# Kernel tuning notes

Hardware: AMD Instinct MI355X
Metric: run time of the kernel (lower is better)

## Reference

```python
import jax, jax.numpy as jnp
import numpy as np

B, T, D = 2, 1024, 2048
N, K, H = 16, 4, 128          # num_heads, num_kv_heads, head_dim
TC = 1024                     # cached tokens
S = TC + T
MAX_WAVELENGTH = 10000.0
BIG_NEG = -2.3819763e38


def _apply_rope(x, positions):
    """RoPE: positions [B,L] applied to x [B,L,heads,H]."""
    half = x.shape[-1] // 2
    freq_exponents = (2.0 / x.shape[-1]) * jnp.arange(half, dtype=jnp.float32)
    timescale = MAX_WAVELENGTH ** freq_exponents                      # [H/2]
    radians = (positions.astype(jnp.float32)[..., None] / timescale)[..., None, :]  # [B,L,1,H/2]
    sin, cos = jnp.sin(radians), jnp.cos(radians)
    x1, x2 = jnp.split(x, 2, axis=-1)
    res = jnp.concatenate([x1 * cos - x2 * sin, x2 * cos + x1 * sin], axis=-1)
    return res.astype(x.dtype)


def setup_inputs() -> dict:
    key = jax.random.key(0)
    ks = jax.random.split(key, 8)
    x = jax.random.normal(ks[0], (B, T, D), dtype=jnp.float32)
    # new tokens sit right after the cache
    positions = jnp.broadcast_to(TC + jnp.arange(T, dtype=jnp.int32), (B, T))
    # causal mask over [cache + new]: query t may attend to keys s <= TC + t
    s_idx = jnp.arange(S)[None, :]
    t_idx = jnp.arange(T)[:, None]
    attn_mask = jnp.broadcast_to((s_idx <= TC + t_idx)[None, None, :, :], (B, 1, T, S))
    cache_k = jax.random.normal(ks[1], (B, TC, K, H), dtype=jnp.float32)
    cache_v = jax.random.normal(ks[2], (B, TC, K, H), dtype=jnp.float32)
    # lecun-normal-ish fan-in scaling (fan_in = D for projections, N*H for output)
    w_q = jax.random.normal(ks[3], (N, D, H), dtype=jnp.float32) * (D ** -0.5)
    w_kv = jax.random.normal(ks[4], (2, K, D, H), dtype=jnp.float32) * (D ** -0.5)
    w_out = jax.random.normal(ks[5], (N, H, D), dtype=jnp.float32) * ((N * H) ** -0.5)
    return {"x": x, "positions": positions, "attn_mask": attn_mask,
            "cache_k": cache_k, "cache_v": cache_v,
            "w_q": w_q, "w_kv": w_kv, "w_out": w_out}


def reference(x, positions, attn_mask, cache_k, cache_v, w_q, w_kv, w_out):
    dtype = x.dtype
    # projections (GQA path: num_kv_heads != num_heads)
    q = jnp.einsum('BTD,NDH->BTNH', x, w_q.astype(dtype))
    kv = jnp.einsum('BSD,CKDH->CBSKH', x, w_kv.astype(dtype))
    k_new, v_new = kv[0], kv[1]
    # inline RoPE + query scaling
    q = _apply_rope(q, positions) * (H ** -0.5)
    k_new = _apply_rope(k_new, positions)
    # KV-cache concat
    k = jnp.concatenate([cache_k, k_new], axis=1)   # [B,S,K,H]
    v = jnp.concatenate([cache_v, v_new], axis=1)
    # group heads: B T (K G) H -> B T K G H
    G = N // K
    qg = q.reshape(q.shape[0], q.shape[1], K, G, H)
    logits = jnp.einsum('BTKGH,BSKH->BKGTS', qg, k,
                        preferred_element_type=jnp.float32)
    masked = jnp.where(attn_mask[:, :, None, :, :], logits, BIG_NEG)
    probs = jax.nn.softmax(masked, axis=-1).astype(dtype)
    enc = jnp.einsum('BKGTS,BSKH->BTKGH', probs, v)
    enc = enc.reshape(enc.shape[0], enc.shape[1], N, H)  # B T (K G) H
    out = jnp.einsum('BTNH,NHD->BTD', enc, w_out.astype(dtype))
    return out, k, v
```

## Files before the change

### kernel.cpp

```cpp
#include <hip/hip_runtime.h>

#define B_  2
#define T_  1024
#define D_  2048
#define NH  16
#define KH  4
#define HD  128
#define TC_ 1024
#define S_  2048

typedef __bf16 bf16x4v __attribute__((ext_vector_type(4)));
typedef __bf16 bf16x8v __attribute__((ext_vector_type(8)));
typedef float  f32x4v  __attribute__((ext_vector_type(4)));

__device__ __forceinline__ void async_copy16(void* lds, const void* g) {
    __builtin_amdgcn_global_load_lds(
        (__attribute__((address_space(1))) void*)g,
        (__attribute__((address_space(3))) void*)lds, 16, 0, 0);
}

__global__ void cvt_x(const float* __restrict__ x, __bf16* __restrict__ xb) {
    int i = (blockIdx.x * 256 + threadIdx.x) * 4;
    float4 v = *(const float4*)(x + i);
    bf16x4v o; o[0]=(__bf16)v.x; o[1]=(__bf16)v.y; o[2]=(__bf16)v.z; o[3]=(__bf16)v.w;
    *(bf16x4v*)(xb + i) = o;
}

__global__ void tp_w(const float* __restrict__ in, __bf16* __restrict__ out) {
    __shared__ float tile[32][33];
    int h0 = blockIdx.x * 32;
    int d0 = blockIdx.y * 32;
    const float* ip = in + (size_t)blockIdx.z * (D_ * HD);
    __bf16* op = out + (size_t)blockIdx.z * (D_ * HD);
    int tx = threadIdx.x, ty = threadIdx.y;
    for (int i = 0; i < 32; i += 8)
        tile[ty + i][tx] = ip[(size_t)(d0 + ty + i) * HD + h0 + tx];
    __syncthreads();
    for (int i = 0; i < 32; i += 8)
        op[(size_t)(h0 + ty + i) * D_ + d0 + tx] = (__bf16)tile[tx][ty + i];
}

__global__ void tp_wout(const float* __restrict__ in, __bf16* __restrict__ out) {
    __shared__ float tile[32][33];
    int d0 = blockIdx.x * 32;
    int h0 = blockIdx.y * 32;
    int n  = blockIdx.z;
    const float* ip = in + (size_t)n * (HD * D_);
    int tx = threadIdx.x, ty = threadIdx.y;
    for (int i = 0; i < 32; i += 8)
        tile[ty + i][tx] = ip[(size_t)(h0 + ty + i) * D_ + d0 + tx];
    __syncthreads();
    for (int i = 0; i < 32; i += 8)
        out[(size_t)(d0 + ty + i) * (NH * HD) + n * HD + h0 + tx] = (__bf16)tile[tx][ty + i];
}

__global__ void tp_v(const float* __restrict__ vout, __bf16* __restrict__ vtb) {
    __shared__ float tile[32][33];
    int z = blockIdx.z; int b = z / KH, kh = z % KH;
    int h0 = blockIdx.x * 32;
    int s0 = blockIdx.y * 32;
    const float* ip = vout + ((size_t)b * S_ * KH + kh) * HD;
    int tx = threadIdx.x, ty = threadIdx.y;
    for (int i = 0; i < 32; i += 8)
        tile[ty + i][tx] = ip[(size_t)(s0 + ty + i) * (KH * HD) + h0 + tx];
    __syncthreads();
    __bf16* op = vtb + ((size_t)b * KH + kh) * (size_t)HD * S_;
    for (int i = 0; i < 32; i += 8)
        op[(size_t)(h0 + ty + i) * S_ + s0 + tx] = (__bf16)tile[tx][ty + i];
}

__global__ void copy_cache(const float4* __restrict__ ck, const float4* __restrict__ cv,
                           float* __restrict__ kout, float* __restrict__ vout,
                           __bf16* __restrict__ kb) {
    int i = blockIdx.x * 256 + threadIdx.x;
    int b = i >> 17;
    int r = i & 131071;
    float4 kv = ck[i];
    ((float4*)(kout + (size_t)b * S_ * KH * HD))[r] = kv;
    ((float4*)(vout + (size_t)b * S_ * KH * HD))[r] = cv[i];
    int h4 = r & 31;
    int kh = (r >> 5) & 3;
    int s  = r >> 7;
    bf16x4v o; o[0]=(__bf16)kv.x; o[1]=(__bf16)kv.y; o[2]=(__bf16)kv.z; o[3]=(__bf16)kv.w;
    *(bf16x4v*)(kb + (((size_t)(b * KH + kh) * S_ + s) * HD) + h4 * 4) = o;
}

__global__ __launch_bounds__(256, 2)
void gemm_bt(const __bf16* __restrict__ A, const __bf16* __restrict__ BT,
             float* __restrict__ C0, float* __restrict__ C1, int ldc, int kchunk) {
    __shared__ __bf16 As[128 * 64];
    __shared__ __bf16 Bs[128 * 64];
    const int m0 = blockIdx.x * 128, n0 = blockIdx.y * 128;
    const int kbeg = blockIdx.z * kchunk;
    float* C = blockIdx.z ? C1 : C0;
    const int tid = threadIdx.x;
    const int wave = tid >> 6, lane = tid & 63;
    const int quad = lane >> 4, l16 = lane & 15;
    const int wm = (wave & 1) * 64, wn = (wave >> 1) * 64;
    const int lrow = lane >> 3;
    const int lsw  = (lane & 7) ^ (lrow & 7);

    f32x4v acc[4][4];
    for (int i = 0; i < 4; i++)
        for (int j = 0; j < 4; j++)
            acc[i][j] = (f32x4v){0.f, 0.f, 0.f, 0.f};

    const __bf16* Abase = A + (size_t)m0 * D_;
    const __bf16* Bbase = BT + (size_t)n0 * D_;

    for (int k0 = kbeg; k0 < kbeg + kchunk; k0 += 64) {
        for (int j = 0; j < 4; j++) {
            int r = wave * 32 + j * 8;
            async_copy16(As + (size_t)r * 64,
                         Abase + (size_t)(r + lrow) * D_ + k0 + lsw * 8);
            async_copy16(Bs + (size_t)r * 64,
                         Bbase + (size_t)(r + lrow) * D_ + k0 + lsw * 8);
        }
        __syncthreads();
        for (int ks = 0; ks < 2; ks++) {
            const int ch = ((ks * 4 + quad) ^ (l16 & 7)) * 8;
            bf16x8v a[4], b[4];
            for (int i = 0; i < 4; i++)
                a[i] = *(const bf16x8v*)(As + (wm + i * 16 + l16) * 64 + ch);
            for (int j = 0; j < 4; j++)
                b[j] = *(const bf16x8v*)(Bs + (wn + j * 16 + l16) * 64 + ch);
            for (int i = 0; i < 4; i++)
                for (int j = 0; j < 4; j++)
                    acc[i][j] = __builtin_amdgcn_mfma_f32_16x16x32_bf16(a[i], b[j], acc[i][j], 0, 0, 0);
        }
        __syncthreads();
    }
    for (int i = 0; i < 4; i++)
        for (int j = 0; j < 4; j++)
            for (int r = 0; r < 4; r++) {
                int row = m0 + wm + i * 16 + quad * 4 + r;
                int col = n0 + wn + j * 16 + l16;
                C[(size_t)row * ldc + col] = acc[i][j][r];
            }
}

__global__ void add2(float* __restrict__ out, const float* __restrict__ p1) {
    int i = blockIdx.x * 256 + threadIdx.x;
    f32x4v a = *(const f32x4v*)(out + (size_t)i * 4);
    f32x4v b = *(const f32x4v*)(p1 + (size_t)i * 4);
    a[0]+=b[0]; a[1]+=b[1]; a[2]+=b[2]; a[3]+=b[3];
    *(f32x4v*)(out + (size_t)i * 4) = a;
}

__global__ void finish_rope(const float* __restrict__ proj, const int* __restrict__ pos,
                            __bf16* __restrict__ qws, float* __restrict__ kout,
                            float* __restrict__ vout, __bf16* __restrict__ kb) {
    const int tau = blockIdx.x;
    const int b = tau >> 10, t = tau & 1023;
    const float p = (float)pos[tau];
    const float* pr  = proj + (size_t)tau * 3072;
    const float* pr2 = pr + (size_t)2048 * 3072;
    const float qscale = 0.08838834764831845f;
    for (int idx = threadIdx.x; idx < (NH + KH) * 64; idx += 256) {
        int head = idx >> 6;
        int hh = idx & 63;
        float ang = p * __expf(-(float)hh * (9.210340371976184f / 64.0f));
        float sn, cs;
        __sincosf(ang, &sn, &cs);
        if (head < NH) {
            float x1 = pr[head * HD + hh]      + pr2[head * HD + hh];
            float x2 = pr[head * HD + hh + 64] + pr2[head * HD + hh + 64];
            size_t qo = ((size_t)tau * NH + head) * HD;
            qws[qo + hh]      = (__bf16)((x1 * cs - x2 * sn) * qscale);
            qws[qo + hh + 64] = (__bf16)((x2 * cs + x1 * sn) * qscale);
        } else {
            int kh = head - NH;
            float x1 = pr[2048 + kh * HD + hh]      + pr2[2048 + kh * HD + hh];
            float x2 = pr[2048 + kh * HD + hh + 64] + pr2[2048 + kh * HD + hh + 64];
            float k1 = x1 * cs - x2 * sn, k2 = x2 * cs + x1 * sn;
            size_t ko = ((size_t)(b * S_ + TC_ + t) * KH + kh) * HD;
            kout[ko + hh]      = k1;
            kout[ko + hh + 64] = k2;
            size_t kbo = ((size_t)(b * KH + kh) * S_ + TC_ + t) * HD;
            kb[kbo + hh]      = (__bf16)k1;
            kb[kbo + hh + 64] = (__bf16)k2;
        }
    }
    for (int idx = threadIdx.x; idx < KH * HD; idx += 256) {
        int kh = idx >> 7, h = idx & 127;
        vout[((size_t)(b * S_ + TC_ + t) * KH + kh) * HD + h] =
            pr[2560 + kh * HD + h] + pr2[2560 + kh * HD + h];
    }
}

__global__ __launch_bounds__(512, 1)
void attn(const __bf16* __restrict__ qws, const __bf16* __restrict__ kb,
          const __bf16* __restrict__ vtb, __bf16* __restrict__ enc) {
    __shared__ __bf16 Qs[128 * 128];
    __shared__ __bf16 Ks[128 * 128];
    __shared__ __bf16 Vs[128 * 128];
    __shared__ __bf16 Ps[128 * 128];

    const int t0 = blockIdx.x * 128;
    const int n  = blockIdx.y;
    const int b  = blockIdx.z;
    const int kh = n / (NH / KH);
    const int tid = threadIdx.x, wave = tid >> 6, lane = tid & 63;
    const int quad = lane >> 4, l16 = lane & 15;
    const int wm = wave * 16;
    const int arow = lane >> 4;
    const int acol = lane & 15;

    {
        const __bf16* qtile = qws + ((size_t)(b * T_ + t0) * NH + n) * HD;
        for (int jj = 0; jj < 4; jj++) {
            int r0 = wm + jj * 4;
            int row = r0 + arow;
            async_copy16(Qs + (size_t)r0 * 128,
                         qtile + (size_t)row * (NH * HD) + ((acol ^ (row & 15)) * 8));
        }
    }

    float m_run[4], l_run[4];
    f32x4v o_acc[8];
    for (int r = 0; r < 4; r++) { m_run[r] = -INFINITY; l_run[r] = 0.f; }
    for (int j = 0; j < 8; j++) o_acc[j] = (f32x4v){0.f, 0.f, 0.f, 0.f};

    const int nS = (TC_ + t0 + 128) >> 7;
    const __bf16* kbase = kb  + ((size_t)(b * KH + kh)) * S_ * HD;
    const __bf16* vbase = vtb + ((size_t)(b * KH + kh)) * (size_t)HD * S_;

    for (int st = 0; st < nS; st++) {
        const int s0 = st * 128;
        {
            const __bf16* ktile = kbase + (size_t)s0 * HD;
            for (int jj = 0; jj < 4; jj++) {
                int r0 = wm + jj * 4;
                int row = r0 + arow;
                async_copy16(Ks + (size_t)r0 * 128,
                             ktile + (size_t)row * HD + ((acol ^ (row & 15)) * 8));
            }
        }
        {
            const __bf16* vtile = vbase + s0;
            for (int jj = 0; jj < 4; jj++) {
                int r0 = wm + jj * 4;
                int row = r0 + arow;
                async_copy16(Vs + (size_t)r0 * 128,
                             vtile + (size_t)row * S_ + ((acol ^ (row & 15)) * 8));
            }
        }
        __syncthreads();

        f32x4v sc[8];
        for (int j = 0; j < 8; j++) sc[j] = (f32x4v){0.f, 0.f, 0.f, 0.f};
        for (int ks = 0; ks < 4; ks++) {
            int ch = (ks * 4 + quad) ^ l16;
            bf16x8v a = *(const bf16x8v*)(Qs + (wm + l16) * 128 + ch * 8);
            bf16x8v bb[8];
            for (int j = 0; j < 8; j++)
                bb[j] = *(const bf16x8v*)(Ks + (j * 16 + l16) * 128 + ch * 8);
            for (int j = 0; j < 8; j++)
                sc[j] = __builtin_amdgcn_mfma_f32_16x16x32_bf16(a, bb[j], sc[j], 0, 0, 0);
        }

        if (st == nS - 1) {
            for (int j = 0; j < 8; j++)
                for (int r = 0; r < 4; r++) {
                    int row = wm + quad * 4 + r;
                    int col = j * 16 + l16;
                    if (col > row) sc[j][r] = -3.0e38f;
                }
        }

        for (int r = 0; r < 4; r++) {
            float mx = sc[0][r];
            for (int j = 1; j < 8; j++) mx = fmaxf(mx, sc[j][r]);
            for (int off = 8; off >= 1; off >>= 1) mx = fmaxf(mx, __shfl_xor(mx, off, 64));
            mx = fmaxf(mx, m_run[r]);
            float alpha = __expf(m_run[r] - mx);
            m_run[r] = mx;
            float s = 0.f;
            for (int j = 0; j < 8; j++) {
                float pv = __expf(sc[j][r] - mx);
                sc[j][r] = pv;
                s += pv;
            }
            for (int off = 8; off >= 1; off >>= 1) s += __shfl_xor(s, off, 64);
            l_run[r] = l_run[r] * alpha + s;
            for (int j = 0; j < 8; j++) o_acc[j][r] *= alpha;
        }

        for (int j = 0; j < 8; j++)
            for (int r = 0; r < 4; r++) {
                int row = wm + quad * 4 + r;
                int c = (j * 2 + (l16 >> 3)) ^ (row & 15);
                Ps[row * 128 + c * 8 + (l16 & 7)] = (__bf16)sc[j][r];
            }
        __syncthreads();

        for (int ks = 0; ks < 4; ks++) {
            int ch = (ks * 4 + quad) ^ l16;
            bf16x8v a = *(const bf16x8v*)(Ps + (wm + l16) * 128 + ch * 8);
            bf16x8v bb[8];
            for (int j = 0; j < 8; j++)
                bb[j] = *(const bf16x8v*)(Vs + (j * 16 + l16) * 128 + ch * 8);
            for (int j = 0; j < 8; j++)
                o_acc[j] = __builtin_amdgcn_mfma_f32_16x16x32_bf16(a, bb[j], o_acc[j], 0, 0, 0);
        }
        __syncthreads();
    }

    for (int r = 0; r < 4; r++) {
        float inv = 1.0f / l_run[r];
        int row = wm + quad * 4 + r;
        for (int j = 0; j < 8; j++) {
            int col = j * 16 + l16;
            enc[((size_t)(b * T_ + t0 + row) * NH + n) * HD + col] =
                (__bf16)(o_acc[j][r] * inv);
        }
    }
}

extern "C" void kernel_launch(void* const* d_in, const int* in_sizes, int n_in,
                              void* d_out, int out_size, void* d_ws, size_t ws_size,
                              hipStream_t stream) {
    const float* x       = (const float*)d_in[0];
    const int*   pos     = (const int*)d_in[1];
    const float* cache_k = (const float*)d_in[3];
    const float* cache_v = (const float*)d_in[4];
    const float* w_q     = (const float*)d_in[5];
    const float* w_kv    = (const float*)d_in[6];
    const float* w_out   = (const float*)d_in[7];

    float* out  = (float*)d_out;
    float* kout = out  + (size_t)B_ * T_ * D_;
    float* vout = kout + (size_t)B_ * S_ * KH * HD;

    char* ws = (char*)d_ws;
    __bf16* xb   = (__bf16*)ws;  ws += (size_t)B_ * T_ * D_ * 2;
    __bf16* wt   = (__bf16*)ws;  ws += (size_t)3072 * D_ * 2;
    __bf16* wot  = (__bf16*)ws;  ws += (size_t)D_ * NH * HD * 2;
    float*  proj = (float*)ws;   ws += (size_t)2 * B_ * T_ * 3072 * 4;
    __bf16* qws  = (__bf16*)ws;  ws += (size_t)B_ * T_ * NH * HD * 2;
    __bf16* kbuf = (__bf16*)ws;  ws += (size_t)B_ * S_ * KH * HD * 2;
    __bf16* vtb  = (__bf16*)ws;  ws += (size_t)B_ * S_ * KH * HD * 2;
    __bf16* enc  = (__bf16*)ws;
    float*  proj1 = proj + (size_t)2048 * 3072;
    float*  op1   = proj;

    cvt_x<<<4096, 256, 0, stream>>>(x, xb);
    tp_w<<<dim3(4, 64, 16), dim3(32, 8), 0, stream>>>(w_q, wt);
    tp_w<<<dim3(4, 64, 8),  dim3(32, 8), 0, stream>>>(w_kv, wt + (size_t)16 * HD * D_);
    tp_wout<<<dim3(64, 4, 16), dim3(32, 8), 0, stream>>>(w_out, wot);
    copy_cache<<<1024, 256, 0, stream>>>((const float4*)cache_k, (const float4*)cache_v, kout, vout, kbuf);
    gemm_bt<<<dim3(16, 24, 2), 256, 0, stream>>>(xb, wt, proj, proj1, 3072, 1024);
    finish_rope<<<2048, 256, 0, stream>>>(proj, pos, qws, kout, vout, kbuf);
    tp_v<<<dim3(4, 64, 8), dim3(32, 8), 0, stream>>>(vout, vtb);
    attn<<<dim3(8, 16, 2), 512, 0, stream>>>(qws, kbuf, vtb, enc);
    gemm_bt<<<dim3(16, 16, 2), 256, 0, stream>>>(enc, wot, out, op1, 2048, 1024);
    add2<<<4096, 256, 0, stream>>>(out, op1);
}
```

Before: 280.0 us.

## Fuse QKV projection GEMM with RoPE epilogue, drop split-K partial buffers

```diff
diff --git a/kernel.cpp b/kernel.cpp
--- a/kernel.cpp
+++ b/kernel.cpp
@@ -86,6 +86,110 @@
 }
 
 __global__ __launch_bounds__(256, 2)
+void gemm_qkv(const __bf16* __restrict__ A, const __bf16* __restrict__ BT,
+              const int* __restrict__ pos, __bf16* __restrict__ qws,
+              float* __restrict__ kout, float* __restrict__ vout,
+              __bf16* __restrict__ kb) {
+    __shared__ __bf16 As[128 * 64];
+    __shared__ __bf16 Bs[128 * 64];
+    const int m0 = blockIdx.x * 128, n0 = blockIdx.y * 128;
+    const int tid = threadIdx.x;
+    const int wave = tid >> 6, lane = tid & 63;
+    const int quad = lane >> 4, l16 = lane & 15;
+    const int wm = (wave & 1) * 64;
+    const int bn0 = (wave >> 1) * 32;
+    const int lrow = lane >> 3;
+    const int lsw  = (lane & 7) ^ (lrow & 7);
+
+    f32x4v acc[4][4];
+    for (int i = 0; i < 4; i++)
+        for (int j = 0; j < 4; j++)
+            acc[i][j] = (f32x4v){0.f, 0.f, 0.f, 0.f};
+
+    const __bf16* Abase = A + (size_t)m0 * D_;
+    const __bf16* Bbase = BT + (size_t)n0 * D_;
+
+    for (int k0 = 0; k0 < D_; k0 += 64) {
+        for (int j = 0; j < 4; j++) {
+            int r = wave * 32 + j * 8;
+            async_copy16(As + (size_t)r * 64,
+                         Abase + (size_t)(r + lrow) * D_ + k0 + lsw * 8);
+            async_copy16(Bs + (size_t)r * 64,
+                         Bbase + (size_t)(r + lrow) * D_ + k0 + lsw * 8);
+        }
+        __syncthreads();
+        for (int ks = 0; ks < 2; ks++) {
+            const int ch = ((ks * 4 + quad) ^ (l16 & 7)) * 8;
+            bf16x8v a[4], b[4];
+            for (int i = 0; i < 4; i++)
+                a[i] = *(const bf16x8v*)(As + (wm + i * 16 + l16) * 64 + ch);
+            for (int j = 0; j < 4; j++) {
+                int bn = bn0 + (j >> 1) * 16 + (j & 1) * 64;
+                b[j] = *(const bf16x8v*)(Bs + (bn + l16) * 64 + ch);
+            }
+            for (int i = 0; i < 4; i++)
+                for (int j = 0; j < 4; j++)
+                    acc[i][j] = __builtin_amdgcn_mfma_f32_16x16x32_bf16(a[i], b[j], acc[i][j], 0, 0, 0);
+        }
+        __syncthreads();
+    }
+
+    const float RFREQ = 9.210340371976184f / 64.0f;
+    const float qscale = 0.08838834764831845f;
+    const int head = blockIdx.y;
+
+    if (head < NH) {
+        for (int i = 0; i < 4; i++)
+            for (int r = 0; r < 4; r++) {
+                int row = m0 + wm + i * 16 + quad * 4 + r;
+                float p = (float)pos[row];
+                size_t qo = ((size_t)row * NH + head) * HD;
+                for (int jp = 0; jp < 2; jp++) {
+                    int hh = bn0 + jp * 16 + l16;
+                    float ang = p * __expf(-(float)hh * RFREQ);
+                    float sn, cs; __sincosf(ang, &sn, &cs);
+                    float x1 = acc[i][jp * 2][r], x2 = acc[i][jp * 2 + 1][r];
+                    qws[qo + hh]      = (__bf16)((x1 * cs - x2 * sn) * qscale);
+                    qws[qo + hh + 64] = (__bf16)((x2 * cs + x1 * sn) * qscale);
+                }
+            }
+    } else if (head < NH + KH) {
+        int kh = head - NH;
+        for (int i = 0; i < 4; i++)
+            for (int r = 0; r < 4; r++) {
+                int row = m0 + wm + i * 16 + quad * 4 + r;
+                int b = row >> 10, t = row & 1023;
+                float p = (float)pos[row];
+                size_t ko  = ((size_t)(b * S_ + TC_ + t) * KH + kh) * HD;
+                size_t kbo = ((size_t)(b * KH + kh) * S_ + TC_ + t) * HD;
+                for (int jp = 0; jp < 2; jp++) {
+                    int hh = bn0 + jp * 16 + l16;
+                    float ang = p * __expf(-(float)hh * RFREQ);
+                    float sn, cs; __sincosf(ang, &sn, &cs);
+                    float x1 = acc[i][jp * 2][r], x2 = acc[i][jp * 2 + 1][r];
+                    float k1 = x1 * cs - x2 * sn, k2 = x2 * cs + x1 * sn;
+                    kout[ko + hh]      = k1;
+                    kout[ko + hh + 64] = k2;
+                    kb[kbo + hh]      = (__bf16)k1;
+                    kb[kbo + hh + 64] = (__bf16)k2;
+                }
+            }
+    } else {
+        int kh = head - NH - KH;
+        for (int i = 0; i < 4; i++)
+            for (int r = 0; r < 4; r++) {
+                int row = m0 + wm + i * 16 + quad * 4 + r;
+                int b = row >> 10, t = row & 1023;
+                size_t vo = ((size_t)(b * S_ + TC_ + t) * KH + kh) * HD;
+                for (int j = 0; j < 4; j++) {
+                    int h = bn0 + (j >> 1) * 16 + (j & 1) * 64 + l16;
+                    vout[vo + h] = acc[i][j][r];
+                }
+            }
+    }
+}
+
+__global__ __launch_bounds__(256, 2)
 void gemm_bt(const __bf16* __restrict__ A, const __bf16* __restrict__ BT,
              float* __restrict__ C0, float* __restrict__ C1, int ldc, int kchunk) {
     __shared__ __bf16 As[128 * 64];
@@ -147,47 +251,6 @@
     *(f32x4v*)(out + (size_t)i * 4) = a;
 }
 
-__global__ void finish_rope(const float* __restrict__ proj, const int* __restrict__ pos,
-                            __bf16* __restrict__ qws, float* __restrict__ kout,
-                            float* __restrict__ vout, __bf16* __restrict__ kb) {
-    const int tau = blockIdx.x;
-    const int b = tau >> 10, t = tau & 1023;
-    const float p = (float)pos[tau];
-    const float* pr  = proj + (size_t)tau * 3072;
-    const float* pr2 = pr + (size_t)2048 * 3072;
-    const float qscale = 0.08838834764831845f;
-    for (int idx = threadIdx.x; idx < (NH + KH) * 64; idx += 256) {
-        int head = idx >> 6;
-        int hh = idx & 63;
-        float ang = p * __expf(-(float)hh * (9.210340371976184f / 64.0f));
-        float sn, cs;
-        __sincosf(ang, &sn, &cs);
-        if (head < NH) {
-            float x1 = pr[head * HD + hh]      + pr2[head * HD + hh];
-            float x2 = pr[head * HD + hh + 64] + pr2[head * HD + hh + 64];
-            size_t qo = ((size_t)tau * NH + head) * HD;
-            qws[qo + hh]      = (__bf16)((x1 * cs - x2 * sn) * qscale);
-            qws[qo + hh + 64] = (__bf16)((x2 * cs + x1 * sn) * qscale);
-        } else {
-            int kh = head - NH;
-            float x1 = pr[2048 + kh * HD + hh]      + pr2[2048 + kh * HD + hh];
-            float x2 = pr[2048 + kh * HD + hh + 64] + pr2[2048 + kh * HD + hh + 64];
-            float k1 = x1 * cs - x2 * sn, k2 = x2 * cs + x1 * sn;
-            size_t ko = ((size_t)(b * S_ + TC_ + t) * KH + kh) * HD;
-            kout[ko + hh]      = k1;
-            kout[ko + hh + 64] = k2;
-            size_t kbo = ((size_t)(b * KH + kh) * S_ + TC_ + t) * HD;
-            kb[kbo + hh]      = (__bf16)k1;
-            kb[kbo + hh + 64] = (__bf16)k2;
-        }
-    }
-    for (int idx = threadIdx.x; idx < KH * HD; idx += 256) {
-        int kh = idx >> 7, h = idx & 127;
-        vout[((size_t)(b * S_ + TC_ + t) * KH + kh) * HD + h] =
-            pr[2560 + kh * HD + h] + pr2[2560 + kh * HD + h];
-    }
-}
-
 __global__ __launch_bounds__(512, 1)
 void attn(const __bf16* __restrict__ qws, const __bf16* __restrict__ kb,
           const __bf16* __restrict__ vtb, __bf16* __restrict__ enc) {
@@ -336,21 +399,18 @@
     __bf16* xb   = (__bf16*)ws;  ws += (size_t)B_ * T_ * D_ * 2;
     __bf16* wt   = (__bf16*)ws;  ws += (size_t)3072 * D_ * 2;
     __bf16* wot  = (__bf16*)ws;  ws += (size_t)D_ * NH * HD * 2;
-    float*  proj = (float*)ws;   ws += (size_t)2 * B_ * T_ * 3072 * 4;
+    float*  op1  = (float*)ws;   ws += (size_t)B_ * T_ * D_ * 4;
     __bf16* qws  = (__bf16*)ws;  ws += (size_t)B_ * T_ * NH * HD * 2;
     __bf16* kbuf = (__bf16*)ws;  ws += (size_t)B_ * S_ * KH * HD * 2;
     __bf16* vtb  = (__bf16*)ws;  ws += (size_t)B_ * S_ * KH * HD * 2;
     __bf16* enc  = (__bf16*)ws;
-    float*  proj1 = proj + (size_t)2048 * 3072;
-    float*  op1   = proj;
 
     cvt_x<<<4096, 256, 0, stream>>>(x, xb);
     tp_w<<<dim3(4, 64, 16), dim3(32, 8), 0, stream>>>(w_q, wt);
     tp_w<<<dim3(4, 64, 8),  dim3(32, 8), 0, stream>>>(w_kv, wt + (size_t)16 * HD * D_);
     tp_wout<<<dim3(64, 4, 16), dim3(32, 8), 0, stream>>>(w_out, wot);
     copy_cache<<<1024, 256, 0, stream>>>((const float4*)cache_k, (const float4*)cache_v, kout, vout, kbuf);
-    gemm_bt<<<dim3(16, 24, 2), 256, 0, stream>>>(xb, wt, proj, proj1, 3072, 1024);
-    finish_rope<<<2048, 256, 0, stream>>>(proj, pos, qws, kout, vout, kbuf);
+    gemm_qkv<<<dim3(16, 24), 256, 0, stream>>>(xb, wt, pos, qws, kout, vout, kbuf);
     tp_v<<<dim3(4, 64, 8), dim3(32, 8), 0, stream>>>(vout, vtb);
     attn<<<dim3(8, 16, 2), 512, 0, stream>>>(qws, kbuf, vtb, enc);
     gemm_bt<<<dim3(16, 16, 2), 256, 0, stream>>>(enc, wot, out, op1, 2048, 1024);
```

New measurement: 274.4 us. 1.02x faster.
